# Optimization experiments

Hardware: AMD Instinct MI355X
Metric: run time of the kernel (lower is better)

The kernel has to match this reference:

```python
import jax, jax.numpy as jnp
import numpy as np

B, T, D, H, C = 128, 1024, 256, 512, 1000

def setup_inputs() -> dict:
    key = jax.random.key(0)
    ks = jax.random.split(key, 16)
    stdv = 1.0 / np.sqrt(H)
    u = lambda k, shape: jax.random.uniform(k, shape, jnp.float32, -stdv, stdv)
    return {
        "x": jax.random.normal(ks[0], (B, T, D), jnp.float32),
        "Wgx": u(ks[1], (D, H)), "Wgh": u(ks[2], (H, H)), "bg": u(ks[3], (H,)),
        "Wix": u(ks[4], (D, H)), "Wih": u(ks[5], (H, H)), "bi": u(ks[6], (H,)),
        "Wfx": u(ks[7], (D, H)), "Wfh": u(ks[8], (H, H)), "bf": u(ks[9], (H,)),
        "Wox": u(ks[10], (D, H)), "Woh": u(ks[11], (H, H)), "bo": u(ks[12], (H,)),
        "Wph": u(ks[13], (H, C)), "bp": u(ks[14], (C,)),
    }

def reference(x, Wgx, Wgh, bg, Wix, Wih, bi, Wfx, Wfh, bf, Wox, Woh, bo, Wph, bp):
    # x: [B, T, D] -> time-major [T, B, D]
    xt = jnp.transpose(x, (1, 0, 2))
    Bsz = x.shape[0]
    Hsz = Wgh.shape[0]
    # Precompute all input projections in one big GEMM per gate (same math as per-step matmul).
    gx = jnp.einsum('tbd,dh->tbh', xt, Wgx)
    ix = jnp.einsum('tbd,dh->tbh', xt, Wix)
    fx = jnp.einsum('tbd,dh->tbh', xt, Wfx)
    ox = jnp.einsum('tbd,dh->tbh', xt, Wox)

    def step(carry, inputs):
        h, c = carry
        gx_t, ix_t, fx_t, ox_t = inputs
        g = jnp.tanh(gx_t + h @ Wgh + bg)
        i = jax.nn.sigmoid(ix_t + h @ Wih + bi)
        f = jax.nn.sigmoid(fx_t + h @ Wfh + bf)
        o = jax.nn.sigmoid(ox_t + h @ Woh + bo)
        c_new = g * i + c * f
        h_new = jnp.tanh(c_new) * o
        return (h_new, c_new), None

    h0 = jnp.zeros((Bsz, Hsz), x.dtype)
    c0 = jnp.zeros((Bsz, Hsz), x.dtype)
    (h_final, _), _ = jax.lax.scan(step, (h0, c0), (gx, ix, fx, ox))
    return h_final @ Wph + bp
```

## Files before the change

### kernel.cpp

```cpp
#include <hip/hip_runtime.h>
#include <stdint.h>

#define B_ 128
#define T_ 1024
#define D_ 256
#define H_ 512
#define C_ 1000
#define GB 8
#define GH 32
#define ROWS 16
#define UN 16
#define KTOT (H_ + D_)
#define NCOL 64
#define LDK (KTOT + 8)
#define TPAD 32

typedef __bf16 bf16x8 __attribute__((ext_vector_type(8)));
typedef float f32x4 __attribute__((ext_vector_type(4)));
typedef unsigned int u32x4 __attribute__((ext_vector_type(4)));

__device__ __forceinline__ uint16_t f2bf(float f) {
  uint32_t u = __float_as_uint(f);
  u += 0x7FFFu + ((u >> 16) & 1u);
  return (uint16_t)(u >> 16);
}
__device__ __forceinline__ float bf2f(uint16_t b) {
  return __uint_as_float(((uint32_t)b) << 16);
}
__device__ __forceinline__ float sigm(float x) { return 1.0f / (1.0f + __expf(-x)); }
__device__ __forceinline__ float tanhfast(float x) { return 2.0f / (1.0f + __expf(-2.0f * x)) - 1.0f; }

__device__ __forceinline__ void load_h2x32_sys(const uint16_t* pA, const uint16_t* pB,
                                               u32x4& a, u32x4& b, u32x4& c, u32x4& d) {
  asm volatile("global_load_dwordx4 %0, %4, off sc0 sc1\n\t"
               "global_load_dwordx4 %1, %4, off offset:16 sc0 sc1\n\t"
               "global_load_dwordx4 %2, %5, off sc0 sc1\n\t"
               "global_load_dwordx4 %3, %5, off offset:16 sc0 sc1\n\t"
               "s_waitcnt vmcnt(0)"
               : "=&v"(a), "=&v"(b), "=&v"(c), "=&v"(d)
               : "v"(pA), "v"(pB) : "memory");
}
__device__ __forceinline__ void store_h16_sys(uint16_t* p, u32x4 v) {
  asm volatile("global_store_dwordx4 %0, %1, off sc0 sc1"
               :: "v"(p), "v"(v) : "memory");
}

__global__ __launch_bounds__(256, 1) void lstm_scan(
    const float* __restrict__ x,
    const float* __restrict__ Wgx, const float* __restrict__ Wgh, const float* __restrict__ bg,
    const float* __restrict__ Wix, const float* __restrict__ Wih, const float* __restrict__ bi,
    const float* __restrict__ Wfx, const float* __restrict__ Wfh, const float* __restrict__ bf_,
    const float* __restrict__ Wox, const float* __restrict__ Woh, const float* __restrict__ bo,
    uint16_t* __restrict__ hring,
    int* __restrict__ tags)
{
  __shared__ __align__(16) uint16_t WtL[NCOL * LDK];
  __shared__ __align__(16) uint16_t AL[ROWS * LDK];
  __shared__ float gbuf[4 * ROWS * UN];
  __shared__ __align__(16) uint16_t hOutL[ROWS * UN];

  const int tid = threadIdx.x;
  const int wg  = blockIdx.x;
  const int bb  = wg & 7;
  const int cg  = wg >> 3;
  const int b0  = bb * ROWS;
  const int u0  = cg * UN;

  const float* Whs[4] = {Wgh, Wih, Wfh, Woh};
  const float* Wxs[4] = {Wgx, Wix, Wfx, Wox};

  {
    const int n    = tid & 63;
    const int kk   = tid >> 6;
    const int gate = n >> 4;
    const int j    = u0 + (n & 15);
    const float* WhP = Whs[gate];
    const float* WxP = Wxs[gate];
    for (int k4 = 0; k4 < KTOT; k4 += 4) {
      int k = k4 + kk;
      float w = (k < H_) ? WhP[(size_t)k * H_ + j] : WxP[(size_t)(k - H_) * H_ + j];
      WtL[n * LDK + k] = f2bf(w);
    }
  }

  const int sr = tid >> 4;
  const int sj = tid & 15;
  const int rr = sr;
  const int uu = sj;

  float c_reg = 0.0f;
  const float bgr = bg[u0 + uu];
  const float bir = bi[u0 + uu];
  const float bfr = bf_[u0 + uu];
  const float bor = bo[u0 + uu];

  {
    uint64_t* zp = (uint64_t*)&AL[sr * LDK + sj * 32];
#pragma unroll
    for (int j = 0; j < 8; ++j) zp[j] = 0ull;
  }

  const int lane = tid & 63;
  const int wv   = tid >> 6;
  const int l15  = lane & 15;
  const int q    = lane >> 4;
  const uint16_t* Abase = &AL[l15 * LDK + q * 8];
  const uint16_t* Bbase = &WtL[(wv * UN + l15) * LDK + q * 8];
  const int* myTag = &tags[(bb * GH + (lane & 31)) * TPAD];

  const size_t SLOT = (size_t)GH * B_ * 16;

  float4 xr0, xr1, xr2, xr3;
  {
    const float* xsrc = x + ((size_t)(b0 + sr) * T_ + 0) * D_ + sj * 16;
    xr0 = ((const float4*)xsrc)[0];
    xr1 = ((const float4*)xsrc)[1];
    xr2 = ((const float4*)xsrc)[2];
    xr3 = ((const float4*)xsrc)[3];
  }

  __syncthreads();

  bf16x8 Bf[6][4];
#pragma unroll
  for (int kk = 0; kk < 6; ++kk) {
#pragma unroll
    for (int j = 0; j < 4; ++j) {
      Bf[kk][j] = *(const bf16x8*)(Bbase + kk * 128 + j * 32);
    }
  }

  for (int t = 0; t < T_; ++t) {
    {
      uint4 o0, o1;
      o0.x = f2bf(xr0.x) | ((uint32_t)f2bf(xr0.y) << 16);
      o0.y = f2bf(xr0.z) | ((uint32_t)f2bf(xr0.w) << 16);
      o0.z = f2bf(xr1.x) | ((uint32_t)f2bf(xr1.y) << 16);
      o0.w = f2bf(xr1.z) | ((uint32_t)f2bf(xr1.w) << 16);
      o1.x = f2bf(xr2.x) | ((uint32_t)f2bf(xr2.y) << 16);
      o1.y = f2bf(xr2.z) | ((uint32_t)f2bf(xr2.w) << 16);
      o1.z = f2bf(xr3.x) | ((uint32_t)f2bf(xr3.y) << 16);
      o1.w = f2bf(xr3.z) | ((uint32_t)f2bf(xr3.w) << 16);
      uint4* xdst = (uint4*)&AL[sr * LDK + H_ + sj * 16];
      xdst[0] = o0; xdst[1] = o1;
    }

    if (t > 0) {
      if (wv == 0) {
        while (true) {
          int v = __hip_atomic_load(myTag, __ATOMIC_RELAXED,
                                    __HIP_MEMORY_SCOPE_SYSTEM);
          if (__ballot(v < t) == 0ull) break;
        }
      }
      __syncthreads();
      const uint16_t* base = hring + (size_t)(t & 1) * SLOT;
      const uint16_t* pA = base + ((2 * sj) * B_ + b0 + sr) * 16;
      const uint16_t* pB = base + ((2 * sj + 1) * B_ + b0 + sr) * 16;
      u32x4 a, b, c, d;
      load_h2x32_sys(pA, pB, a, b, c, d);
      u32x4* adst = (u32x4*)&AL[sr * LDK + sj * 32];
      adst[0] = a; adst[1] = b; adst[2] = c; adst[3] = d;
    }

    {
      const int tn = (t + 1 < T_) ? t + 1 : t;
      const float* xsrc = x + ((size_t)(b0 + sr) * T_ + tn) * D_ + sj * 16;
      xr0 = ((const float4*)xsrc)[0];
      xr1 = ((const float4*)xsrc)[1];
      xr2 = ((const float4*)xsrc)[2];
      xr3 = ((const float4*)xsrc)[3];
    }
    __syncthreads();

    f32x4 a0 = {0.f, 0.f, 0.f, 0.f};
    f32x4 a1 = {0.f, 0.f, 0.f, 0.f};
    f32x4 a2 = {0.f, 0.f, 0.f, 0.f};
    f32x4 a3 = {0.f, 0.f, 0.f, 0.f};
#pragma unroll
    for (int kk = 0; kk < 6; ++kk) {
      const int k0 = kk * 128;
      bf16x8 av0 = *(const bf16x8*)(Abase + k0);
      bf16x8 av1 = *(const bf16x8*)(Abase + k0 + 32);
      bf16x8 av2 = *(const bf16x8*)(Abase + k0 + 64);
      bf16x8 av3 = *(const bf16x8*)(Abase + k0 + 96);
      a0 = __builtin_amdgcn_mfma_f32_16x16x32_bf16(av0, Bf[kk][0], a0, 0, 0, 0);
      a1 = __builtin_amdgcn_mfma_f32_16x16x32_bf16(av1, Bf[kk][1], a1, 0, 0, 0);
      a2 = __builtin_amdgcn_mfma_f32_16x16x32_bf16(av2, Bf[kk][2], a2, 0, 0, 0);
      a3 = __builtin_amdgcn_mfma_f32_16x16x32_bf16(av3, Bf[kk][3], a3, 0, 0, 0);
    }
#pragma unroll
    for (int r = 0; r < 4; ++r) {
      gbuf[wv * (ROWS * UN) + (q * 4 + r) * UN + l15] =
          (a0[r] + a1[r]) + (a2[r] + a3[r]);
    }
    __syncthreads();

    {
      const int o  = rr * UN + uu;
      float pg = gbuf[0 * (ROWS * UN) + o] + bgr;
      float pi = gbuf[1 * (ROWS * UN) + o] + bir;
      float pf = gbuf[2 * (ROWS * UN) + o] + bfr;
      float po = gbuf[3 * (ROWS * UN) + o] + bor;
      float g  = tanhfast(pg);
      float ii = sigm(pi);
      float ff = sigm(pf);
      float oo = sigm(po);
      float c  = g * ii + c_reg * ff;
      c_reg = c;
      float h = tanhfast(c) * oo;
      hOutL[o] = f2bf(h);
    }
    __syncthreads();

    if (tid < 32) {
      u32x4 v = *(const u32x4*)&hOutL[tid * 8];
      uint16_t* dst = hring + (size_t)((t + 1) & 1) * SLOT +
                      ((size_t)cg * B_ + b0) * 16 + tid * 8;
      store_h16_sys(dst, v);
      asm volatile("s_waitcnt vmcnt(0)" ::: "memory");
      if (tid == 0) {
        __hip_atomic_store(&tags[(bb * GH + cg) * TPAD], t + 1,
                           __ATOMIC_RELAXED, __HIP_MEMORY_SCOPE_SYSTEM);
      }
    }
  }
}

__global__ __launch_bounds__(256) void lstm_proj(
    const uint16_t* __restrict__ hfin,
    const float* __restrict__ Wph,
    const float* __restrict__ bp,
    float* __restrict__ out)
{
  __shared__ float hL[8 * H_];
  const int tid = threadIdx.x;
  const int b0  = blockIdx.y * 8;
  const int c   = blockIdx.x * 256 + tid;

  {
    int idx = tid * 16;
#pragma unroll
    for (int e = 0; e < 16; ++e) {
      int i = idx + e;
      int rb = i >> 9, k = i & 511;
      hL[i] = bf2f(hfin[((size_t)(k >> 4) * B_ + b0 + rb) * 16 + (k & 15)]);
    }
  }
  __syncthreads();

  if (c < C_) {
    float acc[8] = {0.f, 0.f, 0.f, 0.f, 0.f, 0.f, 0.f, 0.f};
#pragma unroll 8
    for (int k = 0; k < H_; ++k) {
      float w = Wph[(size_t)k * C_ + c];
#pragma unroll
      for (int rb = 0; rb < 8; ++rb) acc[rb] += hL[rb * H_ + k] * w;
    }
    float bias = bp[c];
#pragma unroll
    for (int rb = 0; rb < 8; ++rb) out[(size_t)(b0 + rb) * C_ + c] = acc[rb] + bias;
  }
}

extern "C" void kernel_launch(void* const* d_in, const int* in_sizes, int n_in,
                              void* d_out, int out_size, void* d_ws, size_t ws_size,
                              hipStream_t stream) {
  const float* x   = (const float*)d_in[0];
  const float* Wgx = (const float*)d_in[1];
  const float* Wgh = (const float*)d_in[2];
  const float* bg  = (const float*)d_in[3];
  const float* Wix = (const float*)d_in[4];
  const float* Wih = (const float*)d_in[5];
  const float* bi  = (const float*)d_in[6];
  const float* Wfx = (const float*)d_in[7];
  const float* Wfh = (const float*)d_in[8];
  const float* bf_ = (const float*)d_in[9];
  const float* Wox = (const float*)d_in[10];
  const float* Woh = (const float*)d_in[11];
  const float* bo  = (const float*)d_in[12];
  const float* Wph = (const float*)d_in[13];
  const float* bp  = (const float*)d_in[14];
  float* out = (float*)d_out;

  uint16_t* hring = (uint16_t*)d_ws;
  int* tags = (int*)((char*)d_ws + (size_t)2 * GH * B_ * 16 * sizeof(uint16_t));

  hipMemsetAsync(tags, 0, GB * GH * TPAD * sizeof(int), stream);

  lstm_scan<<<dim3(GB * GH), dim3(256), 0, stream>>>(
      x, Wgx, Wgh, bg, Wix, Wih, bi, Wfx, Wfh, bf_, Wox, Woh, bo, hring, tags);

  const uint16_t* hfin = hring;
  lstm_proj<<<dim3(4, 16), dim3(256), 0, stream>>>(hfin, Wph, bp, out);
}
```

Before: 2.792 ms.

## Split K across waves, feed h directly from global into MFMA, overlap x-projection

```diff
diff --git a/kernel.cpp b/kernel.cpp
--- a/kernel.cpp
+++ b/kernel.cpp
@@ -13,6 +13,8 @@
 #define KTOT (H_ + D_)
 #define NCOL 64
 #define LDK (KTOT + 8)
+#define LDX (D_ + 8)
+#define GST 17
 #define TPAD 32
 
 typedef __bf16 bf16x8 __attribute__((ext_vector_type(8)));
@@ -30,15 +32,16 @@
 __device__ __forceinline__ float sigm(float x) { return 1.0f / (1.0f + __expf(-x)); }
 __device__ __forceinline__ float tanhfast(float x) { return 2.0f / (1.0f + __expf(-2.0f * x)) - 1.0f; }
 
-__device__ __forceinline__ void load_h2x32_sys(const uint16_t* pA, const uint16_t* pB,
+__device__ __forceinline__ void load_h4x16_sys(const uint16_t* p0, const uint16_t* p1,
+                                               const uint16_t* p2, const uint16_t* p3,
                                                u32x4& a, u32x4& b, u32x4& c, u32x4& d) {
   asm volatile("global_load_dwordx4 %0, %4, off sc0 sc1\n\t"
-               "global_load_dwordx4 %1, %4, off offset:16 sc0 sc1\n\t"
-               "global_load_dwordx4 %2, %5, off sc0 sc1\n\t"
-               "global_load_dwordx4 %3, %5, off offset:16 sc0 sc1\n\t"
+               "global_load_dwordx4 %1, %5, off sc0 sc1\n\t"
+               "global_load_dwordx4 %2, %6, off sc0 sc1\n\t"
+               "global_load_dwordx4 %3, %7, off sc0 sc1\n\t"
                "s_waitcnt vmcnt(0)"
                : "=&v"(a), "=&v"(b), "=&v"(c), "=&v"(d)
-               : "v"(pA), "v"(pB) : "memory");
+               : "v"(p0), "v"(p1), "v"(p2), "v"(p3) : "memory");
 }
 __device__ __forceinline__ void store_h16_sys(uint16_t* p, u32x4 v) {
   asm volatile("global_store_dwordx4 %0, %1, off sc0 sc1"
@@ -55,8 +58,8 @@
     int* __restrict__ tags)
 {
   __shared__ __align__(16) uint16_t WtL[NCOL * LDK];
-  __shared__ __align__(16) uint16_t AL[ROWS * LDK];
-  __shared__ float gbuf[4 * ROWS * UN];
+  __shared__ __align__(16) uint16_t ALx[ROWS * LDX];
+  __shared__ float gpart[4][4][16 * GST];
   __shared__ __align__(16) uint16_t hOutL[ROWS * UN];
 
   const int tid = threadIdx.x;
@@ -94,19 +97,22 @@
   const float bfr = bf_[u0 + uu];
   const float bor = bo[u0 + uu];
 
-  {
-    uint64_t* zp = (uint64_t*)&AL[sr * LDK + sj * 32];
-#pragma unroll
-    for (int j = 0; j < 8; ++j) zp[j] = 0ull;
-  }
-
   const int lane = tid & 63;
   const int wv   = tid >> 6;
   const int l15  = lane & 15;
   const int q    = lane >> 4;
-  const uint16_t* Abase = &AL[l15 * LDK + q * 8];
-  const uint16_t* Bbase = &WtL[(wv * UN + l15) * LDK + q * 8];
+  const uint16_t* AxBase = &ALx[l15 * LDX + q * 8];
   const int* myTag = &tags[(bb * GH + (lane & 31)) * TPAD];
+
+  uint32_t vo0, vo1, vo2, vo3;
+  {
+    const int base_cgp = wv * 8 + (q >> 1);
+    const int e = (q & 1) * 8;
+    vo0 = (uint32_t)((((base_cgp + 0) * B_ + b0 + l15) * 16 + e) * 2);
+    vo1 = (uint32_t)((((base_cgp + 2) * B_ + b0 + l15) * 16 + e) * 2);
+    vo2 = (uint32_t)((((base_cgp + 4) * B_ + b0 + l15) * 16 + e) * 2);
+    vo3 = (uint32_t)((((base_cgp + 6) * B_ + b0 + l15) * 16 + e) * 2);
+  }
 
   const size_t SLOT = (size_t)GH * B_ * 16;
 
@@ -121,13 +127,17 @@
 
   __syncthreads();
 
-  bf16x8 Bf[6][4];
-#pragma unroll
-  for (int kk = 0; kk < 6; ++kk) {
-#pragma unroll
-    for (int j = 0; j < 4; ++j) {
-      Bf[kk][j] = *(const bf16x8*)(Bbase + kk * 128 + j * 32);
-    }
+  bf16x8 Bh[4][4];
+  bf16x8 Bx[4][2];
+#pragma unroll
+  for (int g = 0; g < 4; ++g) {
+    const uint16_t* wrow = &WtL[(g * UN + l15) * LDK + q * 8];
+#pragma unroll
+    for (int j = 0; j < 4; ++j)
+      Bh[g][j] = *(const bf16x8*)(wrow + wv * 128 + j * 32);
+#pragma unroll
+    for (int jx = 0; jx < 2; ++jx)
+      Bx[g][jx] = *(const bf16x8*)(wrow + H_ + wv * 64 + jx * 32);
   }
 
   for (int t = 0; t < T_; ++t) {
@@ -141,8 +151,22 @@
       o1.y = f2bf(xr2.z) | ((uint32_t)f2bf(xr2.w) << 16);
       o1.z = f2bf(xr3.x) | ((uint32_t)f2bf(xr3.y) << 16);
       o1.w = f2bf(xr3.z) | ((uint32_t)f2bf(xr3.w) << 16);
-      uint4* xdst = (uint4*)&AL[sr * LDK + H_ + sj * 16];
+      uint4* xdst = (uint4*)&ALx[sr * LDX + sj * 16];
       xdst[0] = o0; xdst[1] = o1;
+    }
+    __syncthreads();
+
+    f32x4 ag0 = {0.f, 0.f, 0.f, 0.f};
+    f32x4 ag1 = {0.f, 0.f, 0.f, 0.f};
+    f32x4 ag2 = {0.f, 0.f, 0.f, 0.f};
+    f32x4 ag3 = {0.f, 0.f, 0.f, 0.f};
+#pragma unroll
+    for (int jx = 0; jx < 2; ++jx) {
+      bf16x8 ax = *(const bf16x8*)(AxBase + wv * 64 + jx * 32);
+      ag0 = __builtin_amdgcn_mfma_f32_16x16x32_bf16(ax, Bx[0][jx], ag0, 0, 0, 0);
+      ag1 = __builtin_amdgcn_mfma_f32_16x16x32_bf16(ax, Bx[1][jx], ag1, 0, 0, 0);
+      ag2 = __builtin_amdgcn_mfma_f32_16x16x32_bf16(ax, Bx[2][jx], ag2, 0, 0, 0);
+      ag3 = __builtin_amdgcn_mfma_f32_16x16x32_bf16(ax, Bx[3][jx], ag3, 0, 0, 0);
     }
 
     if (t > 0) {
@@ -154,13 +178,34 @@
         }
       }
       __syncthreads();
+
       const uint16_t* base = hring + (size_t)(t & 1) * SLOT;
-      const uint16_t* pA = base + ((2 * sj) * B_ + b0 + sr) * 16;
-      const uint16_t* pB = base + ((2 * sj + 1) * B_ + b0 + sr) * 16;
-      u32x4 a, b, c, d;
-      load_h2x32_sys(pA, pB, a, b, c, d);
-      u32x4* adst = (u32x4*)&AL[sr * LDK + sj * 32];
-      adst[0] = a; adst[1] = b; adst[2] = c; adst[3] = d;
+      u32x4 h0, h1, h2, h3;
+      load_h4x16_sys((const uint16_t*)((const char*)base + vo0),
+                     (const uint16_t*)((const char*)base + vo1),
+                     (const uint16_t*)((const char*)base + vo2),
+                     (const uint16_t*)((const char*)base + vo3),
+                     h0, h1, h2, h3);
+      bf16x8 ah0 = *(const bf16x8*)&h0;
+      bf16x8 ah1 = *(const bf16x8*)&h1;
+      bf16x8 ah2 = *(const bf16x8*)&h2;
+      bf16x8 ah3 = *(const bf16x8*)&h3;
+      ag0 = __builtin_amdgcn_mfma_f32_16x16x32_bf16(ah0, Bh[0][0], ag0, 0, 0, 0);
+      ag1 = __builtin_amdgcn_mfma_f32_16x16x32_bf16(ah0, Bh[1][0], ag1, 0, 0, 0);
+      ag2 = __builtin_amdgcn_mfma_f32_16x16x32_bf16(ah0, Bh[2][0], ag2, 0, 0, 0);
+      ag3 = __builtin_amdgcn_mfma_f32_16x16x32_bf16(ah0, Bh[3][0], ag3, 0, 0, 0);
+      ag0 = __builtin_amdgcn_mfma_f32_16x16x32_bf16(ah1, Bh[0][1], ag0, 0, 0, 0);
+      ag1 = __builtin_amdgcn_mfma_f32_16x16x32_bf16(ah1, Bh[1][1], ag1, 0, 0, 0);
+      ag2 = __builtin_amdgcn_mfma_f32_16x16x32_bf16(ah1, Bh[2][1], ag2, 0, 0, 0);
+      ag3 = __builtin_amdgcn_mfma_f32_16x16x32_bf16(ah1, Bh[3][1], ag3, 0, 0, 0);
+      ag0 = __builtin_amdgcn_mfma_f32_16x16x32_bf16(ah2, Bh[0][2], ag0, 0, 0, 0);
+      ag1 = __builtin_amdgcn_mfma_f32_16x16x32_bf16(ah2, Bh[1][2], ag1, 0, 0, 0);
+      ag2 = __builtin_amdgcn_mfma_f32_16x16x32_bf16(ah2, Bh[2][2], ag2, 0, 0, 0);
+      ag3 = __builtin_amdgcn_mfma_f32_16x16x32_bf16(ah2, Bh[3][2], ag3, 0, 0, 0);
+      ag0 = __builtin_amdgcn_mfma_f32_16x16x32_bf16(ah3, Bh[0][3], ag0, 0, 0, 0);
+      ag1 = __builtin_amdgcn_mfma_f32_16x16x32_bf16(ah3, Bh[1][3], ag1, 0, 0, 0);
+      ag2 = __builtin_amdgcn_mfma_f32_16x16x32_bf16(ah3, Bh[2][3], ag2, 0, 0, 0);
+      ag3 = __builtin_amdgcn_mfma_f32_16x16x32_bf16(ah3, Bh[3][3], ag3, 0, 0, 0);
     }
 
     {
@@ -171,37 +216,23 @@
       xr2 = ((const float4*)xsrc)[2];
       xr3 = ((const float4*)xsrc)[3];
     }
+
+#pragma unroll
+    for (int r = 0; r < 4; ++r) {
+      const int o = (q * 4 + r) * GST + l15;
+      gpart[wv][0][o] = ag0[r];
+      gpart[wv][1][o] = ag1[r];
+      gpart[wv][2][o] = ag2[r];
+      gpart[wv][3][o] = ag3[r];
+    }
     __syncthreads();
 
-    f32x4 a0 = {0.f, 0.f, 0.f, 0.f};
-    f32x4 a1 = {0.f, 0.f, 0.f, 0.f};
-    f32x4 a2 = {0.f, 0.f, 0.f, 0.f};
-    f32x4 a3 = {0.f, 0.f, 0.f, 0.f};
-#pragma unroll
-    for (int kk = 0; kk < 6; ++kk) {
-      const int k0 = kk * 128;
-      bf16x8 av0 = *(const bf16x8*)(Abase + k0);
-      bf16x8 av1 = *(const bf16x8*)(Abase + k0 + 32);
-      bf16x8 av2 = *(const bf16x8*)(Abase + k0 + 64);
-      bf16x8 av3 = *(const bf16x8*)(Abase + k0 + 96);
-      a0 = __builtin_amdgcn_mfma_f32_16x16x32_bf16(av0, Bf[kk][0], a0, 0, 0, 0);
-      a1 = __builtin_amdgcn_mfma_f32_16x16x32_bf16(av1, Bf[kk][1], a1, 0, 0, 0);
-      a2 = __builtin_amdgcn_mfma_f32_16x16x32_bf16(av2, Bf[kk][2], a2, 0, 0, 0);
-      a3 = __builtin_amdgcn_mfma_f32_16x16x32_bf16(av3, Bf[kk][3], a3, 0, 0, 0);
-    }
-#pragma unroll
-    for (int r = 0; r < 4; ++r) {
-      gbuf[wv * (ROWS * UN) + (q * 4 + r) * UN + l15] =
-          (a0[r] + a1[r]) + (a2[r] + a3[r]);
-    }
-    __syncthreads();
-
     {
-      const int o  = rr * UN + uu;
-      float pg = gbuf[0 * (ROWS * UN) + o] + bgr;
-      float pi = gbuf[1 * (ROWS * UN) + o] + bir;
-      float pf = gbuf[2 * (ROWS * UN) + o] + bfr;
-      float po = gbuf[3 * (ROWS * UN) + o] + bor;
+      const int o = rr * GST + uu;
+      float pg = (gpart[0][0][o] + gpart[1][0][o]) + (gpart[2][0][o] + gpart[3][0][o]) + bgr;
+      float pi = (gpart[0][1][o] + gpart[1][1][o]) + (gpart[2][1][o] + gpart[3][1][o]) + bir;
+      float pf = (gpart[0][2][o] + gpart[1][2][o]) + (gpart[2][2][o] + gpart[3][2][o]) + bfr;
+      float po = (gpart[0][3][o] + gpart[1][3][o]) + (gpart[2][3][o] + gpart[3][3][o]) + bor;
       float g  = tanhfast(pg);
       float ii = sigm(pi);
       float ff = sigm(pf);
@@ -209,7 +240,7 @@
       float c  = g * ii + c_reg * ff;
       c_reg = c;
       float h = tanhfast(c) * oo;
-      hOutL[o] = f2bf(h);
+      hOutL[rr * UN + uu] = f2bf(h);
     }
     __syncthreads();
 
```

Result: faster. 2.567 ms (-8.0%).
